# Kernel optimization log

Measured on AMD Instinct MI355X. Metric: run time of the kernel, lower is better.

The kernel has to match this reference:

```python
import jax, jax.numpy as jnp
import numpy as np

D_MODEL = 1024
D_INNER = 4096
K = 127
B, L = 2, 4096

def setup_inputs() -> dict:
    key = jax.random.key(0)
    k1, k2, k3, k4, k5 = jax.random.split(key, 5)
    x = jax.random.normal(k1, (B, L, D_MODEL), dtype=jnp.float32)
    # in_proj: Linear(d, 2*m) -> weight [2m, d] (torch convention)
    w_in = jax.random.normal(k2, (2 * D_INNER, D_MODEL), dtype=jnp.float32) * (1.0 / np.sqrt(D_MODEL))
    # depthwise conv weight: [m, 1, k] in torch; store as [m, k]
    w_dw = jax.random.normal(k3, (D_INNER, K), dtype=jnp.float32) * (1.0 / np.sqrt(K))
    b_dw = jax.random.normal(k4, (D_INNER,), dtype=jnp.float32) * 0.01
    # out_proj: Linear(m, d) -> weight [d, m]
    w_out = jax.random.normal(k5, (D_MODEL, D_INNER), dtype=jnp.float32) * (1.0 / np.sqrt(D_INNER))
    return {"x": x, "w_in": w_in, "w_dw": w_dw, "b_dw": b_dw, "w_out": w_out}

def _causal_dwconv(v, w_dw, b_dw):
    # v: [B, L, m]; causal depthwise conv with kernel K
    # pad K-1 on the left only (equivalent to torch pad=K-1 then [..., :L])
    v_bcl = jnp.transpose(v, (0, 2, 1))  # [B, m, L]
    out = jax.lax.conv_general_dilated(
        v_bcl,
        w_dw[:, None, :],  # [m, 1, K]
        window_strides=(1,),
        padding=[(K - 1, 0)],
        feature_group_count=D_INNER,
        dimension_numbers=("NCH", "OIH", "NCH"),
    )
    out = out + b_dw[None, :, None]
    return jnp.transpose(out, (0, 2, 1))  # [B, L, m]

def reference(x, w_in, w_dw, b_dw, w_out):
    vg = jnp.einsum("bld,ed->ble", x, w_in)  # [B, L, 2m]
    v, g = jnp.split(vg, 2, axis=-1)
    v = _causal_dwconv(v, w_dw, b_dw)
    y = jax.nn.silu(v) * jax.nn.silu(g)
    return jnp.einsum("blm,dm->bld", y, w_out)
```

## Files before the change

### kernel.cpp

```cpp
#include <hip/hip_runtime.h>
#include <hip/hip_bf16.h>
#include <cstdint>
#include <cstddef>

typedef __fp16 f16_t;
typedef __attribute__((ext_vector_type(8))) __fp16 f16x8;
typedef __attribute__((ext_vector_type(4))) __fp16 f16x4;
typedef __attribute__((ext_vector_type(2))) __fp16 h2_t;
typedef __attribute__((ext_vector_type(4))) float floatx4;

__device__ __forceinline__ void async_copy_16B(const void* g, void* l) {
  __builtin_amdgcn_global_load_lds(
      (const __attribute__((address_space(1))) void*)g,
      (__attribute__((address_space(3))) void*)l, 16, 0, 0);
}

__global__ __launch_bounds__(256) void prep(
    const float* __restrict__ x, const float* __restrict__ w_in,
    const float* __restrict__ w_out, const float* __restrict__ w_dw,
    f16_t* __restrict__ x_h, f16_t* __restrict__ wi_h,
    f16_t* __restrict__ wo_h, h2_t* __restrict__ wp) {
  const int tid = blockIdx.x * 256 + threadIdx.x;
  if (tid < 5242880) {
    const float* src;
    f16_t* dst;
    int off;
    if (tid < 2097152) {
      src = x; dst = x_h; off = tid;
    } else if (tid < 4194304) {
      src = w_in; dst = wi_h; off = tid - 2097152;
    } else {
      src = w_out; dst = wo_h; off = tid - 4194304;
    }
    const float4 v = *(const float4*)(src + (size_t)off * 4);
    f16x4 o;
    o.x = (f16_t)v.x; o.y = (f16_t)v.y; o.z = (f16_t)v.z; o.w = (f16_t)v.w;
    *(f16x4*)(dst + (size_t)off * 4) = o;
  } else {
    const int idx = tid - 5242880;
    if (idx < 128 * 4096) {
      const int p = idx >> 12;
      const int c = idx & 4095;
      float a, b;
      if (p < 126) {
        a = w_dw[c * 127 + p]; b = w_dw[c * 127 + p + 1];
      } else if (p == 126) {
        a = w_dw[c * 127 + 126]; b = 0.f;
      } else {
        a = 0.f; b = w_dw[c * 127 + 0];
      }
      h2_t w;
      w.x = (f16_t)a; w.y = (f16_t)b;
      wp[idx] = w;
    }
  }
}

__global__ __launch_bounds__(512, 2) void gemm256_1p(
    const f16_t* __restrict__ A, const f16_t* __restrict__ B,
    f16_t* __restrict__ C, int M, int N, int K) {
  extern __shared__ char smem[];
  const int t = threadIdx.x;
  const int lane = t & 63;
  const int wave = t >> 6;
  const int wm = wave >> 2;
  const int wn = wave & 3;

  const int bid = blockIdx.x;
  const int xcd = bid & 7;
  const int l = bid >> 3;
  const int quad = l >> 5;
  const int qm = (l >> 3) & 3;
  const int qn = l & 7;
  const int m0 = ((xcd >> 1) * 8 + (quad >> 1) * 4 + qm) * 256;
  const int n0 = ((xcd & 1) * 16 + (quad & 1) * 8 + qn) * 256;

  const int fr = lane & 15;
  const int ks = lane >> 4;

  auto stageTile = [&](int d, int k0) {
#pragma unroll
    for (int u = 0; u < 4; ++u) {
      const int q = u * 512 + t;
      const int row = q >> 3, slot = q & 7;
      const int col = (slot ^ (row & 7)) * 8;
      async_copy_16B(A + (size_t)(m0 + row) * K + k0 + col,
                     smem + d * 65536 + row * 128 + slot * 16);
    }
#pragma unroll
    for (int u = 0; u < 4; ++u) {
      const int q = u * 512 + t;
      const int row = q >> 3, slot = q & 7;
      const int col = (slot ^ (row & 7)) * 8;
      async_copy_16B(B + (size_t)(n0 + row) * K + k0 + col,
                     smem + d * 65536 + 32768 + row * 128 + slot * 16);
    }
  };
  auto ldA = [&](int d, int R, int kslot) -> f16x8 {
    return *(const f16x8*)(smem + d * 65536 + R * 128 +
                           ((kslot ^ (R & 7)) << 4));
  };
  auto ldB = [&](int d, int R, int kslot) -> f16x8 {
    return *(const f16x8*)(smem + d * 65536 + 32768 + R * 128 +
                           ((kslot ^ (R & 7)) << 4));
  };

  floatx4 acc[8][4] = {};
  const int kTiles = K / 64;

  stageTile(0, 0);
  for (int tt = 0; tt < kTiles; ++tt) {
    const int d = tt & 1;
    const bool pf = (tt + 1 < kTiles);
    if (pf) {
      stageTile(d ^ 1, (tt + 1) * 64);
      asm volatile("s_waitcnt vmcnt(8)" ::: "memory");
    } else {
      asm volatile("s_waitcnt vmcnt(0)" ::: "memory");
    }
    __builtin_amdgcn_s_barrier();

    f16x8 bf[4][2];
#pragma unroll
    for (int j = 0; j < 4; ++j)
#pragma unroll
      for (int kh = 0; kh < 2; ++kh)
        bf[j][kh] = ldB(d, wn * 64 + j * 16 + fr, kh * 4 + ks);
    __builtin_amdgcn_s_setprio(1);
#pragma unroll
    for (int ii = 0; ii < 8; ++ii) {
      const f16x8 af0 = ldA(d, wm * 128 + ii * 16 + fr, ks);
      const f16x8 af1 = ldA(d, wm * 128 + ii * 16 + fr, 4 + ks);
#pragma unroll
      for (int j = 0; j < 4; ++j)
        acc[ii][j] = __builtin_amdgcn_mfma_f32_16x16x32_f16(
            af0, bf[j][0], acc[ii][j], 0, 0, 0);
#pragma unroll
      for (int j = 0; j < 4; ++j)
        acc[ii][j] = __builtin_amdgcn_mfma_f32_16x16x32_f16(
            af1, bf[j][1], acc[ii][j], 0, 0, 0);
    }
    __builtin_amdgcn_s_setprio(0);
    __builtin_amdgcn_s_barrier();
  }

  const int cr = (lane >> 4) * 4;
  const int cc = lane & 15;
#pragma unroll
  for (int i = 0; i < 8; ++i)
#pragma unroll
    for (int j = 0; j < 4; ++j)
#pragma unroll
      for (int r = 0; r < 4; ++r) {
        const int row = m0 + wm * 128 + i * 16 + cr + r;
        const int col = n0 + wn * 64 + j * 16 + cc;
        C[(size_t)row * N + col] = (f16_t)acc[i][j][r];
      }
}

__global__ __launch_bounds__(512, 2) void gemmN128_1p(
    const f16_t* __restrict__ A, const f16_t* __restrict__ B,
    float* __restrict__ C, int M, int N, int K) {
  extern __shared__ char smem[];
  const int t = threadIdx.x;
  const int lane = t & 63;
  const int wave = t >> 6;
  const int wm = wave >> 2;
  const int wn = wave & 3;

  const int bid = blockIdx.x;
  const int xcd = bid & 7;
  const int l = bid >> 3;
  const int m0 = (xcd * 4 + (l >> 3)) * 256;
  const int n0 = (l & 7) * 128;

  const int fr = lane & 15;
  const int ks = lane >> 4;

  auto stageTile = [&](int d, int k0) {
#pragma unroll
    for (int u = 0; u < 4; ++u) {
      const int q = u * 512 + t;
      const int row = q >> 3, slot = q & 7;
      const int col = (slot ^ (row & 7)) * 8;
      async_copy_16B(A + (size_t)(m0 + row) * K + k0 + col,
                     smem + d * 49152 + row * 128 + slot * 16);
    }
#pragma unroll
    for (int u = 0; u < 2; ++u) {
      const int q = u * 512 + t;
      const int row = q >> 3, slot = q & 7;
      const int col = (slot ^ (row & 7)) * 8;
      async_copy_16B(B + (size_t)(n0 + row) * K + k0 + col,
                     smem + d * 49152 + 32768 + row * 128 + slot * 16);
    }
  };
  auto ldA = [&](int d, int R, int kslot) -> f16x8 {
    return *(const f16x8*)(smem + d * 49152 + R * 128 +
                           ((kslot ^ (R & 7)) << 4));
  };
  auto ldB = [&](int d, int R, int kslot) -> f16x8 {
    return *(const f16x8*)(smem + d * 49152 + 32768 + R * 128 +
                           ((kslot ^ (R & 7)) << 4));
  };

  floatx4 acc[8][2] = {};
  const int kTiles = K / 64;

  stageTile(0, 0);
  for (int tt = 0; tt < kTiles; ++tt) {
    const int d = tt & 1;
    const bool pf = (tt + 1 < kTiles);
    if (pf) {
      stageTile(d ^ 1, (tt + 1) * 64);
      asm volatile("s_waitcnt vmcnt(6)" ::: "memory");
    } else {
      asm volatile("s_waitcnt vmcnt(0)" ::: "memory");
    }
    __builtin_amdgcn_s_barrier();

    f16x8 bf[2][2];
#pragma unroll
    for (int j = 0; j < 2; ++j)
#pragma unroll
      for (int kh = 0; kh < 2; ++kh)
        bf[j][kh] = ldB(d, wn * 32 + j * 16 + fr, kh * 4 + ks);
    __builtin_amdgcn_s_setprio(1);
#pragma unroll
    for (int ii = 0; ii < 8; ++ii) {
      const f16x8 af0 = ldA(d, wm * 128 + ii * 16 + fr, ks);
      const f16x8 af1 = ldA(d, wm * 128 + ii * 16 + fr, 4 + ks);
#pragma unroll
      for (int j = 0; j < 2; ++j)
        acc[ii][j] = __builtin_amdgcn_mfma_f32_16x16x32_f16(
            af0, bf[j][0], acc[ii][j], 0, 0, 0);
#pragma unroll
      for (int j = 0; j < 2; ++j)
        acc[ii][j] = __builtin_amdgcn_mfma_f32_16x16x32_f16(
            af1, bf[j][1], acc[ii][j], 0, 0, 0);
    }
    __builtin_amdgcn_s_setprio(0);
    __builtin_amdgcn_s_barrier();
  }

  const int cr = (lane >> 4) * 4;
  const int cc = lane & 15;
#pragma unroll
  for (int i = 0; i < 8; ++i)
#pragma unroll
    for (int j = 0; j < 2; ++j)
#pragma unroll
      for (int r = 0; r < 4; ++r) {
        const int row = m0 + wm * 128 + i * 16 + cr + r;
        const int col = n0 + wn * 32 + j * 16 + cc;
        C[(size_t)row * N + col] = acc[i][j][r];
      }
}

#define CONV_L 128
#define CPAIRS 127

__global__ __launch_bounds__(256) void conv_gate(
    const f16_t* __restrict__ vg, const h2_t* __restrict__ wp,
    const float* __restrict__ b_dw, f16_t* __restrict__ y) {
  __shared__ uint32_t vtp[CPAIRS * 64];
  __shared__ uint32_t wpl[128 * 64];
  const int t = threadIdx.x;
  const int lane = t & 63;
  const int wave = t >> 6;
  const int c0 = blockIdx.x * 64;
  const int lt = blockIdx.y & 31;
  const int b = blockIdx.y >> 5;
  const int l0 = lt * CONV_L;

#pragma unroll
  for (int it = 0; it < 8; ++it) {
    const int q = it * 256 + t;
    async_copy_16B(wp + (size_t)(q >> 4) * 4096 + c0 + (q & 15) * 4,
                   wpl + q * 4);
  }
  for (int q = t; q < CPAIRS * 8; q += 256) {
    const int m = q >> 3;
    const int oc = (q & 7) * 8;
    const int le = l0 - 126 + 2 * m;
    uint4 a = make_uint4(0u, 0u, 0u, 0u);
    uint4 bb = make_uint4(0u, 0u, 0u, 0u);
    if (le >= 0) {
      const size_t base = (size_t)(b * 4096 + le) * 8192 + c0 + oc;
      a = *(const uint4*)(vg + base);
      bb = *(const uint4*)(vg + base + 8192);
    }
    uint32_t* dst = vtp + m * 64 + oc;
    const uint32_t aw[4] = {a.x, a.y, a.z, a.w};
    const uint32_t bw[4] = {bb.x, bb.y, bb.z, bb.w};
#pragma unroll
    for (int i = 0; i < 4; ++i) {
      dst[2 * i] = (aw[i] & 0xFFFFu) | (bw[i] << 16);
      dst[2 * i + 1] = (aw[i] >> 16) | (bw[i] & 0xFFFF0000u);
    }
  }

  const int c = c0 + lane;
  const int lb = l0 + wave * 32;
  const f16_t* gp = vg + (size_t)(b * 4096 + lb) * 8192 + 4096 + c;
  f16_t gvals[32];
#pragma unroll
  for (int i = 0; i < 32; ++i) gvals[i] = gp[(size_t)i * 8192];

  __syncthreads();

  const float bias = b_dw[c];
  float acc[32];
#pragma unroll
  for (int i = 0; i < 32; ++i) acc[i] = bias;

  const uint32_t* vbase = vtp + wave * 16 * 64 + lane;
  const uint32_t* wbase = wpl + lane;

  h2_t ring[17];
#pragma unroll
  for (int m = 0; m < 17; ++m)
    ring[m] = __builtin_bit_cast(h2_t, vbase[m * 64]);

  {
    const h2_t w0 = __builtin_bit_cast(h2_t, wbase[127 * 64]);
#pragma unroll
    for (int h = 0; h < 16; ++h)
      acc[2 * h + 1] =
          __builtin_amdgcn_fdot2(w0, ring[h], acc[2 * h + 1], false);
  }

#pragma unroll
  for (int k = 0; k < 64; ++k) {
    const h2_t we = __builtin_bit_cast(h2_t, wbase[(2 * k) * 64]);
#pragma unroll
    for (int h = 0; h < 16; ++h)
      acc[2 * h] =
          __builtin_amdgcn_fdot2(we, ring[(k + h) % 17], acc[2 * h], false);
    if (k < 63) {
      const h2_t wo = __builtin_bit_cast(h2_t, wbase[(2 * k + 1) * 64]);
#pragma unroll
      for (int h = 0; h < 16; ++h)
        acc[2 * h + 1] = __builtin_amdgcn_fdot2(wo, ring[(k + 1 + h) % 17],
                                                acc[2 * h + 1], false);
      if (k < 62)
        ring[k % 17] = __builtin_bit_cast(h2_t, vbase[(17 + k) * 64]);
    }
  }

  f16_t* yp = y + (size_t)(b * 4096 + lb) * 4096 + c;
#pragma unroll
  for (int i = 0; i < 32; ++i) {
    const float gv = (float)gvals[i];
    const float v = acc[i];
    const float sv = v / (1.f + __expf(-v));
    const float sg = gv / (1.f + __expf(-gv));
    yp[(size_t)i * 4096] = (f16_t)(sv * sg);
  }
}

extern "C" void kernel_launch(void* const* d_in, const int* in_sizes, int n_in,
                              void* d_out, int out_size, void* d_ws,
                              size_t ws_size, hipStream_t stream) {
  const float* x     = (const float*)d_in[0];
  const float* w_in  = (const float*)d_in[1];
  const float* w_dw  = (const float*)d_in[2];
  const float* b_dw  = (const float*)d_in[3];
  const float* w_out = (const float*)d_in[4];
  float* out = (float*)d_out;

  char* p = (char*)d_ws;
  f16_t* x_h  = (f16_t*)p; p += (size_t)8192 * 1024 * 2;
  f16_t* wi_h = (f16_t*)p; p += (size_t)8192 * 1024 * 2;
  f16_t* wo_h = (f16_t*)p; p += (size_t)1024 * 4096 * 2;
  h2_t*  wp   = (h2_t*)p;  p += (size_t)128 * 4096 * 4;
  f16_t* vg   = (f16_t*)p; p += (size_t)8192 * 8192 * 2;
  f16_t* y    = (f16_t*)p; p += (size_t)8192 * 4096 * 2;

  prep<<<22528, 256, 0, stream>>>(x, w_in, w_out, w_dw, x_h, wi_h, wo_h, wp);

  hipFuncSetAttribute(reinterpret_cast<const void*>(gemm256_1p),
                      hipFuncAttributeMaxDynamicSharedMemorySize, 131072);
  gemm256_1p<<<1024, 512, 131072, stream>>>(x_h, wi_h, vg, 8192, 8192, 1024);

  conv_gate<<<dim3(64, 64), 256, 0, stream>>>(vg, wp, b_dw, y);

  hipFuncSetAttribute(reinterpret_cast<const void*>(gemmN128_1p),
                      hipFuncAttributeMaxDynamicSharedMemorySize, 98304);
  gemmN128_1p<<<256, 512, 98304, stream>>>(y, wo_h, out, 8192, 1024, 4096);
}
```

Before: 444.4 us.

## Deepen GEMM prefetch pipelines and store tiles in fragment-major LDS layout

The input-projection GEMM now uses a 4-deep ring of 32-wide K tiles, and the output GEMM a 3-deep ring of 64-wide K tiles, so more async global-to-LDS copies are in flight. Tiles are written to LDS in MFMA-fragment order, so each lane reads a contiguous 16 bytes without the XOR swizzle. The goal is to hide global load latency better and simplify LDS addressing. The cost is more barriers per K in the first GEMM (half-width tiles) and more LDS in the second (144KB), which may cut occupancy from two blocks to one per CU.

```diff
diff --git a/kernel.cpp b/kernel.cpp
--- a/kernel.cpp
+++ b/kernel.cpp
@@ -56,7 +56,7 @@
   }
 }
 
-__global__ __launch_bounds__(512, 2) void gemm256_1p(
+__global__ __launch_bounds__(512, 2) void gemm256_d4(
     const f16_t* __restrict__ A, const f16_t* __restrict__ B,
     f16_t* __restrict__ C, int M, int N, int K) {
   extern __shared__ char smem[];
@@ -75,70 +75,64 @@
   const int m0 = ((xcd >> 1) * 8 + (quad >> 1) * 4 + qm) * 256;
   const int n0 = ((xcd & 1) * 16 + (quad & 1) * 8 + qn) * 256;
 
-  const int fr = lane & 15;
-  const int ks = lane >> 4;
-
-  auto stageTile = [&](int d, int k0) {
-#pragma unroll
-    for (int u = 0; u < 4; ++u) {
+  auto stageTile = [&](int bf_, int k0) {
+    char* base = smem + bf_ * 32768;
+#pragma unroll
+    for (int u = 0; u < 2; ++u) {
       const int q = u * 512 + t;
-      const int row = q >> 3, slot = q & 7;
-      const int col = (slot ^ (row & 7)) * 8;
-      async_copy_16B(A + (size_t)(m0 + row) * K + k0 + col,
-                     smem + d * 65536 + row * 128 + slot * 16);
-    }
-#pragma unroll
-    for (int u = 0; u < 4; ++u) {
+      const int row = ((q >> 6) << 4) + (q & 15);
+      const int g = (q >> 4) & 3;
+      async_copy_16B(A + (size_t)(m0 + row) * K + k0 + g * 8, base + q * 16);
+    }
+#pragma unroll
+    for (int u = 0; u < 2; ++u) {
       const int q = u * 512 + t;
-      const int row = q >> 3, slot = q & 7;
-      const int col = (slot ^ (row & 7)) * 8;
-      async_copy_16B(B + (size_t)(n0 + row) * K + k0 + col,
-                     smem + d * 65536 + 32768 + row * 128 + slot * 16);
-    }
-  };
-  auto ldA = [&](int d, int R, int kslot) -> f16x8 {
-    return *(const f16x8*)(smem + d * 65536 + R * 128 +
-                           ((kslot ^ (R & 7)) << 4));
-  };
-  auto ldB = [&](int d, int R, int kslot) -> f16x8 {
-    return *(const f16x8*)(smem + d * 65536 + 32768 + R * 128 +
-                           ((kslot ^ (R & 7)) << 4));
+      const int row = ((q >> 6) << 4) + (q & 15);
+      const int g = (q >> 4) & 3;
+      async_copy_16B(B + (size_t)(n0 + row) * K + k0 + g * 8,
+                     base + 16384 + q * 16);
+    }
+  };
+  auto ldA = [&](int bf_, int blk) -> f16x8 {
+    return *(const f16x8*)(smem + bf_ * 32768 + blk * 1024 + lane * 16);
+  };
+  auto ldB = [&](int bf_, int blk) -> f16x8 {
+    return *(const f16x8*)(smem + bf_ * 32768 + 16384 + blk * 1024 +
+                           lane * 16);
   };
 
   floatx4 acc[8][4] = {};
-  const int kTiles = K / 64;
+  const int kT = K / 32;
 
   stageTile(0, 0);
-  for (int tt = 0; tt < kTiles; ++tt) {
-    const int d = tt & 1;
-    const bool pf = (tt + 1 < kTiles);
-    if (pf) {
-      stageTile(d ^ 1, (tt + 1) * 64);
+  stageTile(1, 32);
+  stageTile(2, 64);
+  for (int tt = 0; tt < kT; ++tt) {
+    const int bf_ = tt & 3;
+    const int rem = kT - 1 - tt;
+    if (rem >= 3) {
+      stageTile((tt + 3) & 3, (tt + 3) * 32);
+      asm volatile("s_waitcnt vmcnt(12)" ::: "memory");
+    } else if (rem == 2) {
       asm volatile("s_waitcnt vmcnt(8)" ::: "memory");
+    } else if (rem == 1) {
+      asm volatile("s_waitcnt vmcnt(4)" ::: "memory");
     } else {
       asm volatile("s_waitcnt vmcnt(0)" ::: "memory");
     }
     __builtin_amdgcn_s_barrier();
 
-    f16x8 bf[4][2];
-#pragma unroll
-    for (int j = 0; j < 4; ++j)
-#pragma unroll
-      for (int kh = 0; kh < 2; ++kh)
-        bf[j][kh] = ldB(d, wn * 64 + j * 16 + fr, kh * 4 + ks);
+    f16x8 bfr[4];
+#pragma unroll
+    for (int j = 0; j < 4; ++j) bfr[j] = ldB(bf_, wn * 4 + j);
     __builtin_amdgcn_s_setprio(1);
 #pragma unroll
     for (int ii = 0; ii < 8; ++ii) {
-      const f16x8 af0 = ldA(d, wm * 128 + ii * 16 + fr, ks);
-      const f16x8 af1 = ldA(d, wm * 128 + ii * 16 + fr, 4 + ks);
+      const f16x8 af = ldA(bf_, wm * 8 + ii);
 #pragma unroll
       for (int j = 0; j < 4; ++j)
         acc[ii][j] = __builtin_amdgcn_mfma_f32_16x16x32_f16(
-            af0, bf[j][0], acc[ii][j], 0, 0, 0);
-#pragma unroll
-      for (int j = 0; j < 4; ++j)
-        acc[ii][j] = __builtin_amdgcn_mfma_f32_16x16x32_f16(
-            af1, bf[j][1], acc[ii][j], 0, 0, 0);
+            af, bfr[j], acc[ii][j], 0, 0, 0);
     }
     __builtin_amdgcn_s_setprio(0);
     __builtin_amdgcn_s_barrier();
@@ -158,7 +152,7 @@
       }
 }
 
-__global__ __launch_bounds__(512, 2) void gemmN128_1p(
+__global__ __launch_bounds__(512, 2) void gemmN128_d3(
     const f16_t* __restrict__ A, const f16_t* __restrict__ B,
     float* __restrict__ C, int M, int N, int K) {
   extern __shared__ char smem[];
@@ -174,70 +168,71 @@
   const int m0 = (xcd * 4 + (l >> 3)) * 256;
   const int n0 = (l & 7) * 128;
 
-  const int fr = lane & 15;
-  const int ks = lane >> 4;
-
-  auto stageTile = [&](int d, int k0) {
+  auto stageTile = [&](int bf_, int k0) {
+    char* base = smem + bf_ * 49152;
 #pragma unroll
     for (int u = 0; u < 4; ++u) {
       const int q = u * 512 + t;
-      const int row = q >> 3, slot = q & 7;
-      const int col = (slot ^ (row & 7)) * 8;
-      async_copy_16B(A + (size_t)(m0 + row) * K + k0 + col,
-                     smem + d * 49152 + row * 128 + slot * 16);
+      const int frag = q >> 6;
+      const int row = (frag >> 1) * 16 + (q & 15);
+      const int col = (frag & 1) * 32 + ((q >> 4) & 3) * 8;
+      async_copy_16B(A + (size_t)(m0 + row) * K + k0 + col, base + q * 16);
     }
 #pragma unroll
     for (int u = 0; u < 2; ++u) {
       const int q = u * 512 + t;
-      const int row = q >> 3, slot = q & 7;
-      const int col = (slot ^ (row & 7)) * 8;
+      const int frag = q >> 6;
+      const int row = (frag >> 1) * 16 + (q & 15);
+      const int col = (frag & 1) * 32 + ((q >> 4) & 3) * 8;
       async_copy_16B(B + (size_t)(n0 + row) * K + k0 + col,
-                     smem + d * 49152 + 32768 + row * 128 + slot * 16);
-    }
-  };
-  auto ldA = [&](int d, int R, int kslot) -> f16x8 {
-    return *(const f16x8*)(smem + d * 49152 + R * 128 +
-                           ((kslot ^ (R & 7)) << 4));
-  };
-  auto ldB = [&](int d, int R, int kslot) -> f16x8 {
-    return *(const f16x8*)(smem + d * 49152 + 32768 + R * 128 +
-                           ((kslot ^ (R & 7)) << 4));
+                     base + 32768 + q * 16);
+    }
+  };
+  auto ldA = [&](int bf_, int frag) -> f16x8 {
+    return *(const f16x8*)(smem + bf_ * 49152 + frag * 1024 + lane * 16);
+  };
+  auto ldB = [&](int bf_, int frag) -> f16x8 {
+    return *(const f16x8*)(smem + bf_ * 49152 + 32768 + frag * 1024 +
+                           lane * 16);
   };
 
   floatx4 acc[8][2] = {};
-  const int kTiles = K / 64;
+  const int kT = K / 64;
 
   stageTile(0, 0);
-  for (int tt = 0; tt < kTiles; ++tt) {
-    const int d = tt & 1;
-    const bool pf = (tt + 1 < kTiles);
-    if (pf) {
-      stageTile(d ^ 1, (tt + 1) * 64);
+  stageTile(1, 64);
+  for (int tt = 0; tt < kT; ++tt) {
+    const int bf_ = tt % 3;
+    const int rem = kT - 1 - tt;
+    if (rem >= 2) {
+      stageTile((tt + 2) % 3, (tt + 2) * 64);
+      asm volatile("s_waitcnt vmcnt(12)" ::: "memory");
+    } else if (rem == 1) {
       asm volatile("s_waitcnt vmcnt(6)" ::: "memory");
     } else {
       asm volatile("s_waitcnt vmcnt(0)" ::: "memory");
     }
     __builtin_amdgcn_s_barrier();
 
-    f16x8 bf[2][2];
+    f16x8 bfr[2][2];
 #pragma unroll
     for (int j = 0; j < 2; ++j)
 #pragma unroll
       for (int kh = 0; kh < 2; ++kh)
-        bf[j][kh] = ldB(d, wn * 32 + j * 16 + fr, kh * 4 + ks);
+        bfr[j][kh] = ldB(bf_, (wn * 2 + j) * 2 + kh);
     __builtin_amdgcn_s_setprio(1);
 #pragma unroll
     for (int ii = 0; ii < 8; ++ii) {
-      const f16x8 af0 = ldA(d, wm * 128 + ii * 16 + fr, ks);
-      const f16x8 af1 = ldA(d, wm * 128 + ii * 16 + fr, 4 + ks);
+      const f16x8 af0 = ldA(bf_, (wm * 8 + ii) * 2 + 0);
+      const f16x8 af1 = ldA(bf_, (wm * 8 + ii) * 2 + 1);
 #pragma unroll
       for (int j = 0; j < 2; ++j)
         acc[ii][j] = __builtin_amdgcn_mfma_f32_16x16x32_f16(
-            af0, bf[j][0], acc[ii][j], 0, 0, 0);
+            af0, bfr[j][0], acc[ii][j], 0, 0, 0);
 #pragma unroll
       for (int j = 0; j < 2; ++j)
         acc[ii][j] = __builtin_amdgcn_mfma_f32_16x16x32_f16(
-            af1, bf[j][1], acc[ii][j], 0, 0, 0);
+            af1, bfr[j][1], acc[ii][j], 0, 0, 0);
     }
     __builtin_amdgcn_s_setprio(0);
     __builtin_amdgcn_s_barrier();
@@ -379,13 +374,13 @@
 
   prep<<<22528, 256, 0, stream>>>(x, w_in, w_out, w_dw, x_h, wi_h, wo_h, wp);
 
-  hipFuncSetAttribute(reinterpret_cast<const void*>(gemm256_1p),
+  hipFuncSetAttribute(reinterpret_cast<const void*>(gemm256_d4),
                       hipFuncAttributeMaxDynamicSharedMemorySize, 131072);
-  gemm256_1p<<<1024, 512, 131072, stream>>>(x_h, wi_h, vg, 8192, 8192, 1024);
+  gemm256_d4<<<1024, 512, 131072, stream>>>(x_h, wi_h, vg, 8192, 8192, 1024);
 
   conv_gate<<<dim3(64, 64), 256, 0, stream>>>(vg, wp, b_dw, y);
 
-  hipFuncSetAttribute(reinterpret_cast<const void*>(gemmN128_1p),
-                      hipFuncAttributeMaxDynamicSharedMemorySize, 98304);
-  gemmN128_1p<<<256, 512, 98304, stream>>>(y, wo_h, out, 8192, 1024, 4096);
-}
+  hipFuncSetAttribute(reinterpret_cast<const void*>(gemmN128_d3),
+                      hipFuncAttributeMaxDynamicSharedMemorySize, 147456);
+  gemmN128_d3<<<256, 512, 147456, stream>>>(y, wo_h, out, 8192, 1024, 4096);
+}
```

Result: slower. 485.2 us (+9.2%).
